# Optimization experiments

Hardware: AMD Instinct MI355X
Metric: run time of the kernel (lower is better)

## Reference

```python
import jax, jax.numpy as jnp
import numpy as np

D_MODEL = 1024
N_HEADS = 8
FF_DIM = 4096
B, T = 4, 2048
LN_EPS = 1e-5


def _layernorm(x, g, b):
    m = jnp.mean(x, axis=-1, keepdims=True)
    v = jnp.mean(jnp.square(x - m), axis=-1, keepdims=True)
    return (x - m) / jnp.sqrt(v + LN_EPS) * g + b


def setup_inputs() -> dict:
    key = jax.random.key(0)
    ks = jax.random.split(key, 16)
    s = 1.0 / np.sqrt(D_MODEL)
    sf = 1.0 / np.sqrt(FF_DIM)
    return {
        "x": jax.random.normal(ks[0], (B, T, D_MODEL), dtype=jnp.float32),
        "wq": jax.random.normal(ks[1], (D_MODEL, D_MODEL), dtype=jnp.float32) * s,
        "bq": jnp.zeros((D_MODEL,), jnp.float32),
        "wk": jax.random.normal(ks[2], (D_MODEL, D_MODEL), dtype=jnp.float32) * s,
        "bk": jnp.zeros((D_MODEL,), jnp.float32),
        "wv": jax.random.normal(ks[3], (D_MODEL, D_MODEL), dtype=jnp.float32) * s,
        "bv": jnp.zeros((D_MODEL,), jnp.float32),
        "wo": jax.random.normal(ks[4], (D_MODEL, D_MODEL), dtype=jnp.float32) * s,
        "bo": jnp.zeros((D_MODEL,), jnp.float32),
        "w1": jax.random.normal(ks[5], (D_MODEL, FF_DIM), dtype=jnp.float32) * s,
        "b1": jnp.zeros((FF_DIM,), jnp.float32),
        "w2": jax.random.normal(ks[6], (FF_DIM, D_MODEL), dtype=jnp.float32) * sf,
        "b2": jnp.zeros((D_MODEL,), jnp.float32),
        "g1": jnp.ones((D_MODEL,), jnp.float32),
        "beta1": jnp.zeros((D_MODEL,), jnp.float32),
        "g2": jnp.ones((D_MODEL,), jnp.float32),
        "beta2": jnp.zeros((D_MODEL,), jnp.float32),
    }


def reference(x, wq, bq, wk, bk, wv, bv, wo, bo, w1, b1, w2, b2, g1, beta1, g2, beta2):
    # NOTE: faithful to the torch module — no head reshape; full-D attention
    # with scale sqrt(D // n_heads).
    scale = np.sqrt(D_MODEL // N_HEADS).astype(np.float32)
    q = x @ wq + bq            # [B,T,D]
    k = x @ wk + bk
    v = x @ wv + bv
    scores = jnp.einsum('btd,bsd->bts', q, k) / scale  # [B,T,T]
    attn = jax.nn.softmax(scores, axis=-1)
    ctx = jnp.einsum('bts,bsd->btd', attn, v)
    x = x + (ctx @ wo + bo)
    x = _layernorm(x, g1, beta1)
    x = x + (jax.nn.relu(x @ w1 + b1) @ w2 + b2)
    x = _layernorm(x, g2, beta2)
    return x
```

## Files before the change

kernel.cpp:

```cpp
#include <hip/hip_runtime.h>
#include <hip/hip_bf16.h>
#include <stdint.h>


typedef __bf16 bf16x8 __attribute__((ext_vector_type(8)));
typedef float f32x4 __attribute__((ext_vector_type(4)));

__device__ __forceinline__ unsigned short f2b(float f) {
    __hip_bfloat16 h = __float2bfloat16(f);
    unsigned short u;
    __builtin_memcpy(&u, &h, 2);
    return u;
}

__device__ __forceinline__ void async_copy16(const unsigned short* g, unsigned short* l) {
    __builtin_amdgcn_global_load_lds((__attribute__((address_space(1))) void*)(g),
                                     (__attribute__((address_space(3))) void*)(l),
                                     16, 0, 0);
}

template <int MODE>
__launch_bounds__(256, 2)
__global__ void gemm_bt(const unsigned short* __restrict__ A, int lda,
                        const unsigned short* __restrict__ Bt, int ldb,
                        void* __restrict__ Cv, int ldc,
                        const float* __restrict__ bias,
                        const float* __restrict__ resid, int ldr,
                        int M, int N, int K,
                        long sA, long sB, long sC, long sR, float scale) {
    constexpr bool OUT_BF16  = (MODE == 0 || MODE == 2 || MODE == 4);
    constexpr bool HAS_BIAS  = (MODE == 0 || MODE == 3 || MODE == 4);
    constexpr bool HAS_RESID = (MODE == 3);
    constexpr bool RELU      = (MODE == 4);

    __shared__ unsigned short lds_us[8192];
    unsigned short* ldsA = lds_us;
    unsigned short* ldsB = lds_us + 4096;

    const int nx = (int)gridDim.x, ny = (int)gridDim.y;
    int bx, by;
    if ((ny & 7) == 0) {
        const int n     = (int)blockIdx.y * nx + (int)blockIdx.x;
        const int xcd   = n & 7;
        const int slot  = n >> 3;
        const int bandh = ny >> 3;
        by = xcd * bandh + (slot % bandh);
        bx = slot / bandh;
    } else {
        bx = (int)blockIdx.x;
        by = (int)blockIdx.y;
    }

    const int z = blockIdx.z;
    const unsigned short* Ab = A + (long)z * sA + (long)by * 128 * lda;
    const unsigned short* Bb = Bt + (long)z * sB + (long)bx * 128 * ldb;

    const int tid  = threadIdx.x;
    const int lane = tid & 63;
    const int wid  = tid >> 6;
    const int wr   = wid >> 1;
    const int wc   = wid & 1;

    f32x4 acc[4][4] = {};

    const int p0 = tid, p1 = 256 + tid;
    const int r0 = p0 >> 2, c0 = (((p0 & 3) ^ ((p0 >> 3) & 3))) * 8;
    const int r1 = p1 >> 2, c1 = (((p1 & 3) ^ ((p1 >> 3) & 3))) * 8;
    unsigned short* la0 = ldsA + wid * 512;
    unsigned short* la1 = ldsA + 2048 + wid * 512;
    unsigned short* lb0 = ldsB + wid * 512;
    unsigned short* lb1 = ldsB + 2048 + wid * 512;

    const int kq = lane >> 4;
    const int rr = lane & 15;

    for (int k0 = 0; k0 < K; k0 += 32) {
        __syncthreads();
        async_copy16(Ab + (long)r0 * lda + k0 + c0, la0);
        async_copy16(Ab + (long)r1 * lda + k0 + c1, la1);
        async_copy16(Bb + (long)r0 * ldb + k0 + c0, lb0);
        async_copy16(Bb + (long)r1 * ldb + k0 + c1, lb1);
        __syncthreads();

        bf16x8 af[4], bfr[4];
#pragma unroll
        for (int mi = 0; mi < 4; ++mi) {
            int row = wr * 64 + mi * 16 + rr;
            int ch  = kq ^ ((row >> 1) & 3);
            af[mi]  = *(const bf16x8*)(ldsA + row * 32 + ch * 8);
        }
#pragma unroll
        for (int ni = 0; ni < 4; ++ni) {
            int row = wc * 64 + ni * 16 + rr;
            int ch  = kq ^ ((row >> 1) & 3);
            bfr[ni] = *(const bf16x8*)(ldsB + row * 32 + ch * 8);
        }
#pragma unroll
        for (int mi = 0; mi < 4; ++mi)
#pragma unroll
            for (int ni = 0; ni < 4; ++ni)
                acc[mi][ni] = __builtin_amdgcn_mfma_f32_16x16x32_bf16(af[mi], bfr[ni], acc[mi][ni], 0, 0, 0);
    }

    const long zC = (long)z * sC;
    const int colb = bx * 128 + wc * 64 + rr;
    const int rowb = by * 128 + wr * 64 + kq * 4;
#pragma unroll
    for (int mi = 0; mi < 4; ++mi) {
#pragma unroll
        for (int ni = 0; ni < 4; ++ni) {
            const int col = colb + ni * 16;
            float bv = 0.0f;
            if constexpr (HAS_BIAS) bv = bias[col];
#pragma unroll
            for (int r = 0; r < 4; ++r) {
                const int row = rowb + mi * 16 + r;
                float v = acc[mi][ni][r] * scale + bv;
                if constexpr (HAS_RESID) v += resid[(long)z * sR + (long)row * ldr + col];
                if constexpr (RELU) v = v > 0.0f ? v : 0.0f;
                if constexpr (OUT_BF16)
                    ((unsigned short*)Cv)[zC + (long)row * ldc + col] = f2b(v);
                else
                    ((float*)Cv)[zC + (long)row * ldc + col] = v;
            }
        }
    }
}

__global__ void cast_f32_bf16(const float* __restrict__ in, unsigned short* __restrict__ out, long n) {
    long i = ((long)blockIdx.x * 256 + threadIdx.x) * 4;
    if (i >= n) return;
    float4 v = *(const float4*)(in + i);
    ushort4 o;
    o.x = f2b(v.x); o.y = f2b(v.y); o.z = f2b(v.z); o.w = f2b(v.w);
    *(ushort4*)(out + i) = o;
}

__global__ void concat3(const float* __restrict__ a, const float* __restrict__ b,
                        const float* __restrict__ c, float* __restrict__ o, int n) {
    int i = blockIdx.x * 256 + threadIdx.x;
    if (i < n) { o[i] = a[i]; o[i + n] = b[i]; o[i + 2 * n] = c[i]; }
}

__global__ void transpose_cast(const float* __restrict__ src, unsigned short* __restrict__ dst,
                               int R, int C) {
    __shared__ float tile[32][33];
    const int bx = blockIdx.x * 32;
    const int by = blockIdx.y * 32;
    const int tx = threadIdx.x, ty = threadIdx.y;
#pragma unroll
    for (int i = 0; i < 32; i += 8)
        tile[ty + i][tx] = src[(long)(by + ty + i) * C + bx + tx];
    __syncthreads();
#pragma unroll
    for (int i = 0; i < 32; i += 8)
        dst[(long)(bx + ty + i) * R + by + tx] = f2b(tile[tx][ty + i]);
}

__global__ void transpose_bf16(const unsigned short* __restrict__ src, long sS, int ld,
                               unsigned short* __restrict__ dst, long sD, int R, int C) {
    const int z = blockIdx.z;
    src += (long)z * sS;
    dst += (long)z * sD;
    __shared__ unsigned short tile[32][33];
    const int bx = blockIdx.x * 32;
    const int by = blockIdx.y * 32;
    const int tx = threadIdx.x, ty = threadIdx.y;
#pragma unroll
    for (int i = 0; i < 32; i += 8)
        tile[ty + i][tx] = src[(long)(by + ty + i) * ld + bx + tx];
    __syncthreads();
#pragma unroll
    for (int i = 0; i < 32; i += 8)
        dst[(long)(bx + ty + i) * R + by + tx] = tile[tx][ty + i];
}

__global__ void softmax_rows(const float* __restrict__ S, unsigned short* __restrict__ P) {
    const long row = blockIdx.x;
    const float4* sr = (const float4*)(S + row * 2048);
    const int t = threadIdx.x;
    float4 v0 = sr[t];
    float4 v1 = sr[t + 256];
    float m = fmaxf(fmaxf(fmaxf(v0.x, v0.y), fmaxf(v0.z, v0.w)),
                    fmaxf(fmaxf(v1.x, v1.y), fmaxf(v1.z, v1.w)));
#pragma unroll
    for (int off = 32; off > 0; off >>= 1) m = fmaxf(m, __shfl_down(m, off));
    __shared__ float red[8];
    if ((t & 63) == 0) red[t >> 6] = m;
    __syncthreads();
    m = fmaxf(fmaxf(red[0], red[1]), fmaxf(red[2], red[3]));

    float e0 = __expf(v0.x - m), e1 = __expf(v0.y - m), e2 = __expf(v0.z - m), e3 = __expf(v0.w - m);
    float e4 = __expf(v1.x - m), e5 = __expf(v1.y - m), e6 = __expf(v1.z - m), e7 = __expf(v1.w - m);
    float s = e0 + e1 + e2 + e3 + e4 + e5 + e6 + e7;
#pragma unroll
    for (int off = 32; off > 0; off >>= 1) s += __shfl_down(s, off);
    if ((t & 63) == 0) red[4 + (t >> 6)] = s;
    __syncthreads();
    s = red[4] + red[5] + red[6] + red[7];
    const float inv = 1.0f / s;

    ushort4 o0, o1;
    o0.x = f2b(e0 * inv); o0.y = f2b(e1 * inv); o0.z = f2b(e2 * inv); o0.w = f2b(e3 * inv);
    o1.x = f2b(e4 * inv); o1.y = f2b(e5 * inv); o1.z = f2b(e6 * inv); o1.w = f2b(e7 * inv);
    ushort4* pr = (ushort4*)(P + row * 2048);
    pr[t] = o0;
    pr[t + 256] = o1;
}

template <bool WRITE_BF16>
__global__ void layernorm_rows(const float* in, float* out, unsigned short* outb,
                               const float* __restrict__ g, const float* __restrict__ b) {
    const long row = blockIdx.x;
    const int t = threadIdx.x;
    const float4 v = ((const float4*)(in + row * 1024))[t];
    float s = v.x + v.y + v.z + v.w;
    float q = v.x * v.x + v.y * v.y + v.z * v.z + v.w * v.w;
#pragma unroll
    for (int off = 32; off > 0; off >>= 1) {
        s += __shfl_down(s, off);
        q += __shfl_down(q, off);
    }
    __shared__ float red[8];
    if ((t & 63) == 0) { red[t >> 6] = s; red[4 + (t >> 6)] = q; }
    __syncthreads();
    s = red[0] + red[1] + red[2] + red[3];
    q = red[4] + red[5] + red[6] + red[7];
    const float mean = s * (1.0f / 1024.0f);
    const float var  = q * (1.0f / 1024.0f) - mean * mean;
    const float inv  = rsqrtf(var + 1e-5f);
    const float4 gg = ((const float4*)g)[t];
    const float4 bb = ((const float4*)b)[t];
    float4 o;
    o.x = (v.x - mean) * inv * gg.x + bb.x;
    o.y = (v.y - mean) * inv * gg.y + bb.y;
    o.z = (v.z - mean) * inv * gg.z + bb.z;
    o.w = (v.w - mean) * inv * gg.w + bb.w;
    ((float4*)(out + row * 1024))[t] = o;
    if constexpr (WRITE_BF16) {
        ushort4 ob;
        ob.x = f2b(o.x); ob.y = f2b(o.y); ob.z = f2b(o.z); ob.w = f2b(o.w);
        ((ushort4*)(outb + row * 1024))[t] = ob;
    }
}

extern "C" void kernel_launch(void* const* d_in, const int* in_sizes, int n_in,
                              void* d_out, int out_size, void* d_ws, size_t ws_size,
                              hipStream_t stream) {
    (void)in_sizes; (void)n_in; (void)out_size; (void)ws_size;
    const float* x   = (const float*)d_in[0];
    const float* wq  = (const float*)d_in[1];
    const float* bq  = (const float*)d_in[2];
    const float* wk  = (const float*)d_in[3];
    const float* bk  = (const float*)d_in[4];
    const float* wv  = (const float*)d_in[5];
    const float* bv  = (const float*)d_in[6];
    const float* wo  = (const float*)d_in[7];
    const float* bo  = (const float*)d_in[8];
    const float* w1  = (const float*)d_in[9];
    const float* b1  = (const float*)d_in[10];
    const float* w2  = (const float*)d_in[11];
    const float* b2  = (const float*)d_in[12];
    const float* g1  = (const float*)d_in[13];
    const float* be1 = (const float*)d_in[14];
    const float* g2  = (const float*)d_in[15];
    const float* be2 = (const float*)d_in[16];

    const int D = 1024, FF = 4096, T = 2048, M = 8192;
    const size_t MB = 1ull << 20;
    char* w = (char*)d_ws;
    unsigned short* wqT = (unsigned short*)(w + 0 * MB);
    unsigned short* wkT = (unsigned short*)(w + 2 * MB);
    unsigned short* wvT = (unsigned short*)(w + 4 * MB);
    unsigned short* woT = (unsigned short*)(w + 6 * MB);
    unsigned short* w1T = (unsigned short*)(w + 8 * MB);
    unsigned short* w2T = (unsigned short*)(w + 16 * MB);
    unsigned short* xb  = (unsigned short*)(w + 24 * MB);
    unsigned short* qkv = (unsigned short*)(w + 40 * MB);
    float*          bcat = (float*)(w + 88 * MB);
    unsigned short* vT  = (unsigned short*)(w + 88 * MB);
    float*          sc  = (float*)(w + 104 * MB);
    unsigned short* pr  = (unsigned short*)(w + 168 * MB);
    unsigned short* ctxb = (unsigned short*)(w + 104 * MB);
    float*          t0  = (float*)(w + 168 * MB);
    unsigned short* x1b = (unsigned short*)(w + 40 * MB);
    unsigned short* h   = (unsigned short*)(w + 104 * MB);
    float*          y   = (float*)(w + 56 * MB);

    const dim3 tb(32, 8);
    transpose_cast<<<dim3(32, 32), tb, 0, stream>>>(wq, wqT, D, D);
    transpose_cast<<<dim3(32, 32), tb, 0, stream>>>(wk, wkT, D, D);
    transpose_cast<<<dim3(32, 32), tb, 0, stream>>>(wv, wvT, D, D);
    transpose_cast<<<dim3(32, 32), tb, 0, stream>>>(wo, woT, D, D);
    transpose_cast<<<dim3(128, 32), tb, 0, stream>>>(w1, w1T, D, FF);
    transpose_cast<<<dim3(32, 128), tb, 0, stream>>>(w2, w2T, FF, D);
    concat3<<<4, 256, 0, stream>>>(bq, bk, bv, bcat, D);
    cast_f32_bf16<<<8192, 256, 0, stream>>>(x, xb, (long)M * D);

    gemm_bt<0><<<dim3(24, 64, 1), 256, 0, stream>>>(xb, D, wqT, D, qkv, 3 * D, bcat, nullptr, 0,
                                                    M, 3 * D, D, 0, 0, 0, 0, 1.0f);

    transpose_bf16<<<dim3(32, 64, 4), tb, 0, stream>>>(qkv + 2 * D, (long)T * 3 * D, 3 * D,
                                                       vT, (long)D * T, T, D);

    gemm_bt<1><<<dim3(16, 16, 4), 256, 0, stream>>>(qkv, 3 * D, qkv + D, 3 * D, sc, T,
                                                    nullptr, nullptr, 0, T, T, D,
                                                    (long)T * 3 * D, (long)T * 3 * D, (long)T * T, 0,
                                                    0.08838834764831845f);
    softmax_rows<<<8192, 256, 0, stream>>>(sc, pr);

    gemm_bt<2><<<dim3(8, 16, 4), 256, 0, stream>>>(pr, T, vT, T, ctxb, D,
                                                   nullptr, nullptr, 0, T, D, T,
                                                   (long)T * T, (long)D * T, (long)T * D, 0, 1.0f);

    gemm_bt<3><<<dim3(8, 64, 1), 256, 0, stream>>>(ctxb, D, woT, D, t0, D, bo, x, D,
                                                   M, D, D, 0, 0, 0, 0, 1.0f);

    layernorm_rows<true><<<8192, 256, 0, stream>>>(t0, t0, x1b, g1, be1);

    gemm_bt<4><<<dim3(32, 64, 1), 256, 0, stream>>>(x1b, D, w1T, D, h, FF, b1, nullptr, 0,
                                                    M, FF, D, 0, 0, 0, 0, 1.0f);
    gemm_bt<3><<<dim3(8, 64, 1), 256, 0, stream>>>(h, FF, w2T, FF, y, D, b2, t0, D,
                                                   M, D, FF, 0, 0, 0, 0, 1.0f);

    layernorm_rows<false><<<8192, 256, 0, stream>>>(y, (float*)d_out, nullptr, g2, be2);
}
```

Baseline: 572.7 us.

## Double GEMM K-tile to 64 with 8-way XOR swizzle; batch weight transposes

The shared bf16 GEMM now stages 64-wide K slices (16 KB per operand tile pair, 32 KB total LDS) with a new 8-chunk XOR swizzle, and runs two MFMA sub-steps per barrier pair. This halves the number of __syncthreads and load rounds per output tile across all GEMMs. The four square weight transposes are merged into one launch writing contiguous transposed buffers. Doubling LDS per block may reduce occupancy below the two blocks per CU requested in launch bounds.

Result: faster. 515.2 us (-10.0%).

```diff
diff --git a/kernel.cpp b/kernel.cpp
--- a/kernel.cpp
+++ b/kernel.cpp
@@ -33,9 +33,9 @@
     constexpr bool HAS_RESID = (MODE == 3);
     constexpr bool RELU      = (MODE == 4);
 
-    __shared__ unsigned short lds_us[8192];
+    __shared__ unsigned short lds_us[16384];
     unsigned short* ldsA = lds_us;
-    unsigned short* ldsB = lds_us + 4096;
+    unsigned short* ldsB = lds_us + 8192;
 
     const int nx = (int)gridDim.x, ny = (int)gridDim.y;
     int bx, by;
@@ -63,43 +63,50 @@
 
     f32x4 acc[4][4] = {};
 
-    const int p0 = tid, p1 = 256 + tid;
-    const int r0 = p0 >> 2, c0 = (((p0 & 3) ^ ((p0 >> 3) & 3))) * 8;
-    const int r1 = p1 >> 2, c1 = (((p1 & 3) ^ ((p1 >> 3) & 3))) * 8;
-    unsigned short* la0 = ldsA + wid * 512;
-    unsigned short* la1 = ldsA + 2048 + wid * 512;
-    unsigned short* lb0 = ldsB + wid * 512;
-    unsigned short* lb1 = ldsB + 2048 + wid * 512;
+    long offA[4], offB[4];
+    unsigned short* dA[4];
+    unsigned short* dB[4];
+#pragma unroll
+    for (int p = 0; p < 4; ++p) {
+        const int s = p * 256 + tid;
+        const int r = s >> 3;
+        const int c = ((s & 7) ^ (r & 7)) * 8;
+        offA[p] = (long)r * lda + c;
+        offB[p] = (long)r * ldb + c;
+        dA[p] = ldsA + (p * 256 + wid * 64) * 8;
+        dB[p] = ldsB + (p * 256 + wid * 64) * 8;
+    }
 
     const int kq = lane >> 4;
     const int rr = lane & 15;
-
-    for (int k0 = 0; k0 < K; k0 += 32) {
+    const int st0 = kq ^ (rr & 7);
+    const int st1 = (4 + kq) ^ (rr & 7);
+
+    for (int k0 = 0; k0 < K; k0 += 64) {
         __syncthreads();
-        async_copy16(Ab + (long)r0 * lda + k0 + c0, la0);
-        async_copy16(Ab + (long)r1 * lda + k0 + c1, la1);
-        async_copy16(Bb + (long)r0 * ldb + k0 + c0, lb0);
-        async_copy16(Bb + (long)r1 * ldb + k0 + c1, lb1);
+#pragma unroll
+        for (int p = 0; p < 4; ++p) {
+            async_copy16(Ab + offA[p] + k0, dA[p]);
+            async_copy16(Bb + offB[p] + k0, dB[p]);
+        }
         __syncthreads();
 
-        bf16x8 af[4], bfr[4];
-#pragma unroll
-        for (int mi = 0; mi < 4; ++mi) {
-            int row = wr * 64 + mi * 16 + rr;
-            int ch  = kq ^ ((row >> 1) & 3);
-            af[mi]  = *(const bf16x8*)(ldsA + row * 32 + ch * 8);
+#pragma unroll
+        for (int ks = 0; ks < 2; ++ks) {
+            const int st = ks ? st1 : st0;
+            bf16x8 af[4], bfr[4];
+#pragma unroll
+            for (int mi = 0; mi < 4; ++mi)
+                af[mi] = *(const bf16x8*)(ldsA + (wr * 64 + mi * 16 + rr) * 64 + st * 8);
+#pragma unroll
+            for (int ni = 0; ni < 4; ++ni)
+                bfr[ni] = *(const bf16x8*)(ldsB + (wc * 64 + ni * 16 + rr) * 64 + st * 8);
+#pragma unroll
+            for (int mi = 0; mi < 4; ++mi)
+#pragma unroll
+                for (int ni = 0; ni < 4; ++ni)
+                    acc[mi][ni] = __builtin_amdgcn_mfma_f32_16x16x32_bf16(af[mi], bfr[ni], acc[mi][ni], 0, 0, 0);
         }
-#pragma unroll
-        for (int ni = 0; ni < 4; ++ni) {
-            int row = wc * 64 + ni * 16 + rr;
-            int ch  = kq ^ ((row >> 1) & 3);
-            bfr[ni] = *(const bf16x8*)(ldsB + row * 32 + ch * 8);
-        }
-#pragma unroll
-        for (int mi = 0; mi < 4; ++mi)
-#pragma unroll
-            for (int ni = 0; ni < 4; ++ni)
-                acc[mi][ni] = __builtin_amdgcn_mfma_f32_16x16x32_bf16(af[mi], bfr[ni], acc[mi][ni], 0, 0, 0);
     }
 
     const long zC = (long)z * sC;
@@ -155,6 +162,24 @@
 #pragma unroll
     for (int i = 0; i < 32; i += 8)
         dst[(long)(bx + ty + i) * R + by + tx] = f2b(tile[tx][ty + i]);
+}
+
+__global__ void transpose_cast4(const float* __restrict__ s0, const float* __restrict__ s1,
+                                const float* __restrict__ s2, const float* __restrict__ s3,
+                                unsigned short* __restrict__ dst, int N) {
+    const float* src = (blockIdx.z == 0) ? s0 : (blockIdx.z == 1) ? s1 : (blockIdx.z == 2) ? s2 : s3;
+    unsigned short* d = dst + (long)blockIdx.z * N * N;
+    __shared__ float tile[32][33];
+    const int bx = blockIdx.x * 32;
+    const int by = blockIdx.y * 32;
+    const int tx = threadIdx.x, ty = threadIdx.y;
+#pragma unroll
+    for (int i = 0; i < 32; i += 8)
+        tile[ty + i][tx] = src[(long)(by + ty + i) * N + bx + tx];
+    __syncthreads();
+#pragma unroll
+    for (int i = 0; i < 32; i += 8)
+        d[(long)(bx + ty + i) * N + by + tx] = f2b(tile[tx][ty + i]);
 }
 
 __global__ void transpose_bf16(const unsigned short* __restrict__ src, long sS, int ld,
@@ -270,8 +295,6 @@
     const size_t MB = 1ull << 20;
     char* w = (char*)d_ws;
     unsigned short* wqT = (unsigned short*)(w + 0 * MB);
-    unsigned short* wkT = (unsigned short*)(w + 2 * MB);
-    unsigned short* wvT = (unsigned short*)(w + 4 * MB);
     unsigned short* woT = (unsigned short*)(w + 6 * MB);
     unsigned short* w1T = (unsigned short*)(w + 8 * MB);
     unsigned short* w2T = (unsigned short*)(w + 16 * MB);
@@ -288,10 +311,7 @@
     float*          y   = (float*)(w + 56 * MB);
 
     const dim3 tb(32, 8);
-    transpose_cast<<<dim3(32, 32), tb, 0, stream>>>(wq, wqT, D, D);
-    transpose_cast<<<dim3(32, 32), tb, 0, stream>>>(wk, wkT, D, D);
-    transpose_cast<<<dim3(32, 32), tb, 0, stream>>>(wv, wvT, D, D);
-    transpose_cast<<<dim3(32, 32), tb, 0, stream>>>(wo, woT, D, D);
+    transpose_cast4<<<dim3(32, 32, 4), tb, 0, stream>>>(wq, wk, wv, wo, wqT, D);
     transpose_cast<<<dim3(128, 32), tb, 0, stream>>>(w1, w1T, D, FF);
     transpose_cast<<<dim3(32, 128), tb, 0, stream>>>(w2, w2T, FF, D);
     concat3<<<4, 256, 0, stream>>>(bq, bk, bv, bcat, D);
```
